# Kernel tuning notes

Measured on AMD Instinct MI355X. Metric: run time of the kernel, lower is better.

The kernel has to match this reference:

```python
import jax, jax.numpy as jnp
import numpy as np

EPS = 1e-16


def setup_inputs() -> dict:
    key = jax.random.key(0)
    k1, k2 = jax.random.split(key)
    p = jax.random.normal(k1, (2, 32, 2048, 4), dtype=jnp.float32)
    q = jax.random.normal(k2, (32, 2048, 4), dtype=jnp.float32)
    return {"p": p, "q": q}


def reference(p, q):
    # im=False path: take the real part of the complex generated momenta
    p_real = p[0]                      # (B, N, 4)
    # loss_norm_choice='p3', take_sqrt=True: use 3-momenta (drop energy)
    p3 = p_real[..., 1:]               # (B, N, 3)
    q3 = q[..., 1:]                    # (B, M, 3)
    # Pairwise Euclidean distance (cdist) via the expanded quadratic form to
    # avoid materializing the (B, N, M, 3) difference tensor.
    x2 = jnp.sum(p3 * p3, axis=-1)     # (B, N)
    y2 = jnp.sum(q3 * q3, axis=-1)     # (B, M)
    xy = jnp.einsum('bnd,bmd->bnm', p3, q3)  # (B, N, M)
    dist_sq = x2[..., :, None] + y2[..., None, :] - 2.0 * xy
    dist = jnp.sqrt(jnp.maximum(dist_sq, 0.0) + EPS)  # (B, N, M)
    # Bidirectional nearest-neighbor min-reduction
    min_pq = jnp.min(dist, axis=-1)    # (B, N)
    min_qp = jnp.min(dist, axis=-2)    # (B, M)
    chamfer_loss = jnp.sum((min_pq + min_qp) * 0.5)
    return chamfer_loss
```

## Files before the change

### kernel.cpp

```cpp
#include <hip/hip_runtime.h>
#include <math.h>


#define NPTS   2048
#define NBATCH 32
#define NTOT   (2 * NBATCH * NPTS)
#define EPSF   1e-16f
#define BIGF   3.4e38f

__device__ __forceinline__ float min3f(float a, float b, float c) {
    return fminf(fminf(a, b), c);
}

__global__ __launch_bounds__(256) void chamfer_tile_kernel(
    const float* __restrict__ P, const float* __restrict__ Q,
    unsigned int* __restrict__ ws)
{
    __shared__ float4 sp[256];
    __shared__ float4 sq[256];
    __shared__ float  scol[4][256];

    const int tid = threadIdx.x;
    const int tx  = tid & 15;
    const int ty  = tid >> 4;
    const int bi  = blockIdx.x;
    const int bj  = blockIdx.y;
    const int b   = blockIdx.z;

    {
        float4 pv = ((const float4*)P)[(size_t)b * NPTS + bi * 256 + tid];
        sp[tid] = make_float4(pv.y, pv.z, pv.w,
                              pv.y*pv.y + pv.z*pv.z + pv.w*pv.w);
        float4 qv = ((const float4*)Q)[(size_t)b * NPTS + bj * 256 + tid];
        sq[tid] = make_float4(-2.f*qv.y, -2.f*qv.z, -2.f*qv.w,
                              qv.y*qv.y + qv.z*qv.z + qv.w*qv.w);
    }
    __syncthreads();

    float px[16], py[16], pz[16], x2[16];
    #pragma unroll
    for (int k = 0; k < 16; ++k) {
        float4 v = sp[ty + 16 * k];
        px[k] = v.x; py[k] = v.y; pz[k] = v.z; x2[k] = v.w;
    }

    float rowacc[16], colacc[16];
    #pragma unroll
    for (int k = 0; k < 16; ++k) { rowacc[k] = BIGF; colacc[k] = BIGF; }

    for (int jp = 0; jp < 8; ++jp) {
        float4 q0 = sq[tx + 32 * jp];
        float4 q1 = sq[tx + 32 * jp + 16];
        float c0 = BIGF, c1 = BIGF;
        #pragma unroll
        for (int k = 0; k < 16; k += 2) {
            float t00 = fmaf(px[k],   q0.x, fmaf(py[k],   q0.y, pz[k]   * q0.z));
            float t01 = fmaf(px[k],   q1.x, fmaf(py[k],   q1.y, pz[k]   * q1.z));
            float t10 = fmaf(px[k+1], q0.x, fmaf(py[k+1], q0.y, pz[k+1] * q0.z));
            float t11 = fmaf(px[k+1], q1.x, fmaf(py[k+1], q1.y, pz[k+1] * q1.z));
            rowacc[k]   = min3f(rowacc[k],   t00 + q0.w, t01 + q1.w);
            rowacc[k+1] = min3f(rowacc[k+1], t10 + q0.w, t11 + q1.w);
            c0 = min3f(c0, t00 + x2[k], t10 + x2[k+1]);
            c1 = min3f(c1, t01 + x2[k], t11 + x2[k+1]);
        }
        colacc[2*jp]     = c0;
        colacc[2*jp + 1] = c1;
    }

    #pragma unroll
    for (int k = 0; k < 16; ++k) {
        float v = rowacc[k];
        v = fminf(v, __shfl_xor(v, 1));
        v = fminf(v, __shfl_xor(v, 2));
        v = fminf(v, __shfl_xor(v, 4));
        v = fminf(v, __shfl_xor(v, 8));
        rowacc[k] = v;
    }
    if (tx == 0) {
        #pragma unroll
        for (int k = 0; k < 16; ++k) {
            float d2 = fmaxf(x2[k] + rowacc[k], 0.f);
            atomicMin(&ws[b * NPTS + bi * 256 + (ty + 16 * k)],
                      __float_as_uint(d2));
        }
    }

    #pragma unroll
    for (int j = 0; j < 16; ++j) {
        float v = colacc[j];
        v = fminf(v, __shfl_xor(v, 16));
        v = fminf(v, __shfl_xor(v, 32));
        colacc[j] = v;
    }
    {
        const int wv   = tid >> 6;
        const int lane = tid & 63;
        if (lane < 16) {
            #pragma unroll
            for (int j = 0; j < 16; ++j) scol[wv][j * 16 + lane] = colacc[j];
        }
    }
    __syncthreads();
    {
        const int c = tid;
        float v = fminf(fminf(scol[0][c], scol[1][c]),
                        fminf(scol[2][c], scol[3][c]));
        float d2 = fmaxf(v + sq[c].w, 0.f);
        atomicMin(&ws[NBATCH * NPTS + b * NPTS + bj * 256 + c],
                  __float_as_uint(d2));
    }
}

__global__ __launch_bounds__(256) void chamfer_sum_kernel(
    const unsigned int* __restrict__ ws, float* __restrict__ out)
{
    __shared__ float rbuf[4];
    const int tid = threadIdx.x;
    const int i0  = blockIdx.x * 256 + tid;

    float s = 0.f;
    for (int i = i0; i < NTOT; i += gridDim.x * 256)
        s += sqrtf(__uint_as_float(ws[i]) + EPSF);

    #pragma unroll
    for (int off = 32; off > 0; off >>= 1) s += __shfl_down(s, off);
    if ((tid & 63) == 0) rbuf[tid >> 6] = s;
    __syncthreads();
    if (tid == 0)
        atomicAdd(out, 0.5f * ((rbuf[0] + rbuf[1]) + (rbuf[2] + rbuf[3])));
}

extern "C" void kernel_launch(void* const* d_in, const int* in_sizes, int n_in,
                              void* d_out, int out_size, void* d_ws, size_t ws_size,
                              hipStream_t stream) {
    const float* P = (const float*)d_in[0];
    const float* Q = (const float*)d_in[1];
    float* out = (float*)d_out;
    unsigned int* ws = (unsigned int*)d_ws;

    hipMemsetAsync(ws, 0x7F, (size_t)NTOT * sizeof(unsigned int), stream);
    hipMemsetAsync(out, 0, sizeof(float), stream);

    dim3 grid(NPTS / 256, NPTS / 256, NBATCH);
    chamfer_tile_kernel<<<grid, 256, 0, stream>>>(P, Q, ws);

    chamfer_sum_kernel<<<128, 256, 0, stream>>>(ws, out);
}
```

Baseline: 83.04 us.

## Stream all Q chunks per row block and replace atomics with partial-min buffers

Each block now owns 128 P rows and loops over all eight 256-point Q chunks with double-buffered shared memory. Row minima complete inside the block, so the row sqrt and sum happen in-kernel. Column minima go to a per-wave partial buffer without atomics, and a finish kernel reduces them and adds the row partial sums. This drops the workspace memset and the atomicMin traffic, at the cost of fewer blocks (512 instead of 2048), a serial loop per block, and a larger workspace read in the finish step.

```diff
diff --git a/kernel.cpp b/kernel.cpp
--- a/kernel.cpp
+++ b/kernel.cpp
@@ -4,7 +4,10 @@
 
 #define NPTS   2048
 #define NBATCH 32
-#define NTOT   (2 * NBATCH * NPTS)
+#define ROWCH  128
+#define NBI    (NPTS / ROWCH)
+#define NQCH   (NPTS / 256)
+#define COLPART_FLOATS ((size_t)NBATCH * NBI * 4 * NPTS)
 #define EPSF   1e-16f
 #define BIGF   3.4e38f
 
@@ -12,115 +15,130 @@
     return fminf(fminf(a, b), c);
 }
 
-__global__ __launch_bounds__(256) void chamfer_tile_kernel(
+__global__ __launch_bounds__(256) void chamfer_main_kernel(
     const float* __restrict__ P, const float* __restrict__ Q,
-    unsigned int* __restrict__ ws)
+    float* __restrict__ ws)
 {
-    __shared__ float4 sp[256];
-    __shared__ float4 sq[256];
-    __shared__ float  scol[4][256];
+    __shared__ float4 sq[2][256];
+    __shared__ float  rsum[4];
 
-    const int tid = threadIdx.x;
-    const int tx  = tid & 15;
-    const int ty  = tid >> 4;
-    const int bi  = blockIdx.x;
-    const int bj  = blockIdx.y;
-    const int b   = blockIdx.z;
+    const int tid  = threadIdx.x;
+    const int tx   = tid & 15;
+    const int ty   = tid >> 4;
+    const int lane = tid & 63;
+    const int wv   = tid >> 6;
+    const int bi   = blockIdx.x;
+    const int b    = blockIdx.y;
 
+    const float4* Pb = (const float4*)P + (size_t)b * NPTS + (size_t)bi * ROWCH;
+    float px[8], py[8], pz[8], x2[8], rowacc[8];
+    #pragma unroll
+    for (int k = 0; k < 8; ++k) {
+        float4 v = Pb[ty + 16 * k];
+        px[k] = v.y; py[k] = v.z; pz[k] = v.w;
+        x2[k] = v.y * v.y + v.z * v.z + v.w * v.w;
+        rowacc[k] = BIGF;
+    }
+
+    const float4* Qb = (const float4*)Q + (size_t)b * NPTS;
     {
-        float4 pv = ((const float4*)P)[(size_t)b * NPTS + bi * 256 + tid];
-        sp[tid] = make_float4(pv.y, pv.z, pv.w,
-                              pv.y*pv.y + pv.z*pv.z + pv.w*pv.w);
-        float4 qv = ((const float4*)Q)[(size_t)b * NPTS + bj * 256 + tid];
-        sq[tid] = make_float4(-2.f*qv.y, -2.f*qv.z, -2.f*qv.w,
-                              qv.y*qv.y + qv.z*qv.z + qv.w*qv.w);
+        float4 qv = Qb[tid];
+        sq[0][tid] = make_float4(-2.f * qv.y, -2.f * qv.z, -2.f * qv.w,
+                                 qv.y * qv.y + qv.z * qv.z + qv.w * qv.w);
     }
     __syncthreads();
 
-    float px[16], py[16], pz[16], x2[16];
-    #pragma unroll
-    for (int k = 0; k < 16; ++k) {
-        float4 v = sp[ty + 16 * k];
-        px[k] = v.x; py[k] = v.y; pz[k] = v.z; x2[k] = v.w;
+    float* colbase = ws + (((size_t)b * NBI + bi) * 4 + wv) * NPTS;
+
+    for (int jc = 0; jc < NQCH; ++jc) {
+        const int cur = jc & 1;
+        const bool have = (jc + 1 < NQCH);
+        float4 qnext;
+        if (have) qnext = Qb[(jc + 1) * 256 + tid];
+
+        float colv[16];
+        #pragma unroll
+        for (int jp = 0; jp < 8; ++jp) {
+            float4 q0 = sq[cur][tx + 32 * jp];
+            float4 q1 = sq[cur][tx + 32 * jp + 16];
+            float c0 = BIGF, c1 = BIGF;
+            #pragma unroll
+            for (int k = 0; k < 8; k += 2) {
+                float t00 = fmaf(px[k],   q0.x, fmaf(py[k],   q0.y, pz[k]   * q0.z));
+                float t01 = fmaf(px[k],   q1.x, fmaf(py[k],   q1.y, pz[k]   * q1.z));
+                float t10 = fmaf(px[k+1], q0.x, fmaf(py[k+1], q0.y, pz[k+1] * q0.z));
+                float t11 = fmaf(px[k+1], q1.x, fmaf(py[k+1], q1.y, pz[k+1] * q1.z));
+                rowacc[k]   = min3f(rowacc[k],   t00 + q0.w, t01 + q1.w);
+                rowacc[k+1] = min3f(rowacc[k+1], t10 + q0.w, t11 + q1.w);
+                c0 = min3f(c0, t00 + x2[k], t10 + x2[k+1]);
+                c1 = min3f(c1, t01 + x2[k], t11 + x2[k+1]);
+            }
+            colv[2*jp]     = c0;
+            colv[2*jp + 1] = c1;
+        }
+
+        #pragma unroll
+        for (int j = 0; j < 16; ++j) {
+            float v = colv[j];
+            v = fminf(v, __shfl_xor(v, 16));
+            v = fminf(v, __shfl_xor(v, 32));
+            colv[j] = v;
+        }
+        if (lane < 16) {
+            #pragma unroll
+            for (int j = 0; j < 16; ++j)
+                colbase[jc * 256 + j * 16 + lane] = colv[j];
+        }
+
+        if (have) {
+            sq[cur ^ 1][tid] = make_float4(
+                -2.f * qnext.y, -2.f * qnext.z, -2.f * qnext.w,
+                qnext.y * qnext.y + qnext.z * qnext.z + qnext.w * qnext.w);
+        }
+        __syncthreads();
     }
 
-    float rowacc[16], colacc[16];
+    float rs = 0.f;
     #pragma unroll
-    for (int k = 0; k < 16; ++k) { rowacc[k] = BIGF; colacc[k] = BIGF; }
-
-    for (int jp = 0; jp < 8; ++jp) {
-        float4 q0 = sq[tx + 32 * jp];
-        float4 q1 = sq[tx + 32 * jp + 16];
-        float c0 = BIGF, c1 = BIGF;
-        #pragma unroll
-        for (int k = 0; k < 16; k += 2) {
-            float t00 = fmaf(px[k],   q0.x, fmaf(py[k],   q0.y, pz[k]   * q0.z));
-            float t01 = fmaf(px[k],   q1.x, fmaf(py[k],   q1.y, pz[k]   * q1.z));
-            float t10 = fmaf(px[k+1], q0.x, fmaf(py[k+1], q0.y, pz[k+1] * q0.z));
-            float t11 = fmaf(px[k+1], q1.x, fmaf(py[k+1], q1.y, pz[k+1] * q1.z));
-            rowacc[k]   = min3f(rowacc[k],   t00 + q0.w, t01 + q1.w);
-            rowacc[k+1] = min3f(rowacc[k+1], t10 + q0.w, t11 + q1.w);
-            c0 = min3f(c0, t00 + x2[k], t10 + x2[k+1]);
-            c1 = min3f(c1, t01 + x2[k], t11 + x2[k+1]);
-        }
-        colacc[2*jp]     = c0;
-        colacc[2*jp + 1] = c1;
-    }
-
-    #pragma unroll
-    for (int k = 0; k < 16; ++k) {
+    for (int k = 0; k < 8; ++k) {
         float v = rowacc[k];
         v = fminf(v, __shfl_xor(v, 1));
         v = fminf(v, __shfl_xor(v, 2));
         v = fminf(v, __shfl_xor(v, 4));
         v = fminf(v, __shfl_xor(v, 8));
-        rowacc[k] = v;
+        rs += sqrtf(fmaxf(x2[k] + v, 0.f) + EPSF);
     }
-    if (tx == 0) {
-        #pragma unroll
-        for (int k = 0; k < 16; ++k) {
-            float d2 = fmaxf(x2[k] + rowacc[k], 0.f);
-            atomicMin(&ws[b * NPTS + bi * 256 + (ty + 16 * k)],
-                      __float_as_uint(d2));
-        }
-    }
-
-    #pragma unroll
-    for (int j = 0; j < 16; ++j) {
-        float v = colacc[j];
-        v = fminf(v, __shfl_xor(v, 16));
-        v = fminf(v, __shfl_xor(v, 32));
-        colacc[j] = v;
-    }
-    {
-        const int wv   = tid >> 6;
-        const int lane = tid & 63;
-        if (lane < 16) {
-            #pragma unroll
-            for (int j = 0; j < 16; ++j) scol[wv][j * 16 + lane] = colacc[j];
-        }
-    }
+    if (tx != 0) rs = 0.f;
+    rs += __shfl_xor(rs, 16);
+    rs += __shfl_xor(rs, 32);
+    if (lane == 0) rsum[wv] = rs;
     __syncthreads();
-    {
-        const int c = tid;
-        float v = fminf(fminf(scol[0][c], scol[1][c]),
-                        fminf(scol[2][c], scol[3][c]));
-        float d2 = fmaxf(v + sq[c].w, 0.f);
-        atomicMin(&ws[NBATCH * NPTS + b * NPTS + bj * 256 + c],
-                  __float_as_uint(d2));
-    }
+    if (tid == 0)
+        ws[COLPART_FLOATS + (size_t)b * NBI + bi] =
+            (rsum[0] + rsum[1]) + (rsum[2] + rsum[3]);
 }
 
-__global__ __launch_bounds__(256) void chamfer_sum_kernel(
-    const unsigned int* __restrict__ ws, float* __restrict__ out)
+__global__ __launch_bounds__(256) void chamfer_finish_kernel(
+    const float* __restrict__ ws, const float* __restrict__ Q,
+    float* __restrict__ out)
 {
     __shared__ float rbuf[4];
     const int tid = threadIdx.x;
-    const int i0  = blockIdx.x * 256 + tid;
+    const int b   = blockIdx.x >> 3;
+    const int cc  = blockIdx.x & 7;
+    const int col = cc * 256 + tid;
 
-    float s = 0.f;
-    for (int i = i0; i < NTOT; i += gridDim.x * 256)
-        s += sqrtf(__uint_as_float(ws[i]) + EPSF);
+    const float* base = ws + (size_t)b * NBI * 4 * NPTS + col;
+    float v = BIGF;
+    #pragma unroll
+    for (int i = 0; i < NBI * 4; ++i)
+        v = fminf(v, base[(size_t)i * NPTS]);
+
+    float4 qv = ((const float4*)Q)[(size_t)b * NPTS + col];
+    float y2 = qv.y * qv.y + qv.z * qv.z + qv.w * qv.w;
+    float s = sqrtf(fmaxf(v + y2, 0.f) + EPSF);
+
+    if (tid < 2) s += ws[COLPART_FLOATS + (size_t)blockIdx.x * 2 + tid];
 
     #pragma unroll
     for (int off = 32; off > 0; off >>= 1) s += __shfl_down(s, off);
@@ -136,13 +154,10 @@
     const float* P = (const float*)d_in[0];
     const float* Q = (const float*)d_in[1];
     float* out = (float*)d_out;
-    unsigned int* ws = (unsigned int*)d_ws;
+    float* ws  = (float*)d_ws;
 
-    hipMemsetAsync(ws, 0x7F, (size_t)NTOT * sizeof(unsigned int), stream);
     hipMemsetAsync(out, 0, sizeof(float), stream);
-
-    dim3 grid(NPTS / 256, NPTS / 256, NBATCH);
-    chamfer_tile_kernel<<<grid, 256, 0, stream>>>(P, Q, ws);
-
-    chamfer_sum_kernel<<<128, 256, 0, stream>>>(ws, out);
+    dim3 g1(NBI, NBATCH);
+    chamfer_main_kernel<<<g1, 256, 0, stream>>>(P, Q, ws);
+    chamfer_finish_kernel<<<256, 256, 0, stream>>>(ws, Q, out);
 }
```

Result: slower. 94.36 us (+13.6%).

## Replace atomicMin workspace with per-tile partial minima and smaller P tiles

Applied to the files above, without the earlier changes.

The tile kernel now covers 128 P rows by 256 Q columns, so the grid grows to 16x8x32 blocks. It writes per-tile partial row and column minima to distinct workspace slots instead of doing atomicMin into a shared array, which removes the workspace memset and the atomic traffic. P is loaded straight from global memory into registers, with no shared staging. The finish kernel then reduces the partials across tiles before the sqrt and sum. The cost is a larger workspace and extra reads in the finish kernel, and each thread now holds half as many P rows, which may lower register reuse per Q load.

```diff
diff --git a/kernel.cpp b/kernel.cpp
--- a/kernel.cpp
+++ b/kernel.cpp
@@ -4,7 +4,9 @@
 
 #define NPTS   2048
 #define NBATCH 32
-#define NTOT   (2 * NBATCH * NPTS)
+#define NBI    16
+#define NBJ    8
+#define WS_ROW_FLOATS ((size_t)NBATCH * NBI * NBJ * 128)
 #define EPSF   1e-16f
 #define BIGF   3.4e38f
 
@@ -14,46 +16,46 @@
 
 __global__ __launch_bounds__(256) void chamfer_tile_kernel(
     const float* __restrict__ P, const float* __restrict__ Q,
-    unsigned int* __restrict__ ws)
+    float* __restrict__ ws)
 {
-    __shared__ float4 sp[256];
     __shared__ float4 sq[256];
     __shared__ float  scol[4][256];
+    __shared__ float  rrow[128];
 
-    const int tid = threadIdx.x;
-    const int tx  = tid & 15;
-    const int ty  = tid >> 4;
-    const int bi  = blockIdx.x;
-    const int bj  = blockIdx.y;
-    const int b   = blockIdx.z;
+    const int tid  = threadIdx.x;
+    const int tx   = tid & 15;
+    const int ty   = tid >> 4;
+    const int lane = tid & 63;
+    const int wv   = tid >> 6;
+    const int bi   = blockIdx.x;
+    const int bj   = blockIdx.y;
+    const int b    = blockIdx.z;
 
     {
-        float4 pv = ((const float4*)P)[(size_t)b * NPTS + bi * 256 + tid];
-        sp[tid] = make_float4(pv.y, pv.z, pv.w,
-                              pv.y*pv.y + pv.z*pv.z + pv.w*pv.w);
         float4 qv = ((const float4*)Q)[(size_t)b * NPTS + bj * 256 + tid];
-        sq[tid] = make_float4(-2.f*qv.y, -2.f*qv.z, -2.f*qv.w,
-                              qv.y*qv.y + qv.z*qv.z + qv.w*qv.w);
+        sq[tid] = make_float4(-2.f * qv.y, -2.f * qv.z, -2.f * qv.w,
+                              qv.y * qv.y + qv.z * qv.z + qv.w * qv.w);
+    }
+
+    const float4* Pb = (const float4*)P + (size_t)b * NPTS + (size_t)bi * 128;
+    float px[8], py[8], pz[8], x2[8], rowacc[8];
+    #pragma unroll
+    for (int k = 0; k < 8; ++k) {
+        float4 v = Pb[ty + 16 * k];
+        px[k] = v.y; py[k] = v.z; pz[k] = v.w;
+        x2[k] = v.y * v.y + v.z * v.z + v.w * v.w;
+        rowacc[k] = BIGF;
     }
     __syncthreads();
 
-    float px[16], py[16], pz[16], x2[16];
+    float colacc[16];
     #pragma unroll
-    for (int k = 0; k < 16; ++k) {
-        float4 v = sp[ty + 16 * k];
-        px[k] = v.x; py[k] = v.y; pz[k] = v.z; x2[k] = v.w;
-    }
-
-    float rowacc[16], colacc[16];
-    #pragma unroll
-    for (int k = 0; k < 16; ++k) { rowacc[k] = BIGF; colacc[k] = BIGF; }
-
     for (int jp = 0; jp < 8; ++jp) {
         float4 q0 = sq[tx + 32 * jp];
         float4 q1 = sq[tx + 32 * jp + 16];
         float c0 = BIGF, c1 = BIGF;
         #pragma unroll
-        for (int k = 0; k < 16; k += 2) {
+        for (int k = 0; k < 8; k += 2) {
             float t00 = fmaf(px[k],   q0.x, fmaf(py[k],   q0.y, pz[k]   * q0.z));
             float t01 = fmaf(px[k],   q1.x, fmaf(py[k],   q1.y, pz[k]   * q1.z));
             float t10 = fmaf(px[k+1], q0.x, fmaf(py[k+1], q0.y, pz[k+1] * q0.z));
@@ -68,21 +70,13 @@
     }
 
     #pragma unroll
-    for (int k = 0; k < 16; ++k) {
+    for (int k = 0; k < 8; ++k) {
         float v = rowacc[k];
         v = fminf(v, __shfl_xor(v, 1));
         v = fminf(v, __shfl_xor(v, 2));
         v = fminf(v, __shfl_xor(v, 4));
         v = fminf(v, __shfl_xor(v, 8));
-        rowacc[k] = v;
-    }
-    if (tx == 0) {
-        #pragma unroll
-        for (int k = 0; k < 16; ++k) {
-            float d2 = fmaxf(x2[k] + rowacc[k], 0.f);
-            atomicMin(&ws[b * NPTS + bi * 256 + (ty + 16 * k)],
-                      __float_as_uint(d2));
-        }
+        if (tx == 0) rrow[ty + 16 * k] = x2[k] + v;
     }
 
     #pragma unroll
@@ -92,35 +86,50 @@
         v = fminf(v, __shfl_xor(v, 32));
         colacc[j] = v;
     }
-    {
-        const int wv   = tid >> 6;
-        const int lane = tid & 63;
-        if (lane < 16) {
-            #pragma unroll
-            for (int j = 0; j < 16; ++j) scol[wv][j * 16 + lane] = colacc[j];
-        }
+    if (lane < 16) {
+        #pragma unroll
+        for (int j = 0; j < 16; ++j) scol[wv][j * 16 + lane] = colacc[j];
     }
     __syncthreads();
+
     {
-        const int c = tid;
-        float v = fminf(fminf(scol[0][c], scol[1][c]),
-                        fminf(scol[2][c], scol[3][c]));
-        float d2 = fmaxf(v + sq[c].w, 0.f);
-        atomicMin(&ws[NBATCH * NPTS + b * NPTS + bj * 256 + c],
-                  __float_as_uint(d2));
+        float v = fminf(fminf(scol[0][tid], scol[1][tid]),
+                        fminf(scol[2][tid], scol[3][tid]));
+        float* wsC = ws + WS_ROW_FLOATS;
+        wsC[(((size_t)b * NBJ + bj) * NBI + bi) * 256 + tid] = v + sq[tid].w;
+    }
+    if (tid < 128) {
+        ws[(((size_t)b * NBI + bi) * NBJ + bj) * 128 + tid] = rrow[tid];
     }
 }
 
-__global__ __launch_bounds__(256) void chamfer_sum_kernel(
-    const unsigned int* __restrict__ ws, float* __restrict__ out)
+__global__ __launch_bounds__(256) void chamfer_finish_kernel(
+    const float* __restrict__ ws, float* __restrict__ out)
 {
     __shared__ float rbuf[4];
     const int tid = threadIdx.x;
-    const int i0  = blockIdx.x * 256 + tid;
+    const int i   = blockIdx.x * 256 + tid;
+    const int b   = i >> 11;
+    const int e   = i & 2047;
 
-    float s = 0.f;
-    for (int i = i0; i < NTOT; i += gridDim.x * 256)
-        s += sqrtf(__uint_as_float(ws[i]) + EPSF);
+    float s;
+    {
+        const int bi = e >> 7, rl = e & 127;
+        const float* rb = ws + ((size_t)(b * NBI + bi) * NBJ) * 128 + rl;
+        float v = BIGF;
+        #pragma unroll
+        for (int j = 0; j < NBJ; ++j) v = fminf(v, rb[j * 128]);
+        s = sqrtf(fmaxf(v, 0.f) + EPSF);
+    }
+    {
+        const int bj = e >> 8, cl = e & 255;
+        const float* cb = ws + WS_ROW_FLOATS
+                        + ((size_t)(b * NBJ + bj) * NBI) * 256 + cl;
+        float v = BIGF;
+        #pragma unroll
+        for (int j = 0; j < NBI; ++j) v = fminf(v, cb[j * 256]);
+        s += sqrtf(fmaxf(v, 0.f) + EPSF);
+    }
 
     #pragma unroll
     for (int off = 32; off > 0; off >>= 1) s += __shfl_down(s, off);
@@ -136,13 +145,10 @@
     const float* P = (const float*)d_in[0];
     const float* Q = (const float*)d_in[1];
     float* out = (float*)d_out;
-    unsigned int* ws = (unsigned int*)d_ws;
+    float* ws  = (float*)d_ws;
 
-    hipMemsetAsync(ws, 0x7F, (size_t)NTOT * sizeof(unsigned int), stream);
     hipMemsetAsync(out, 0, sizeof(float), stream);
-
-    dim3 grid(NPTS / 256, NPTS / 256, NBATCH);
+    dim3 grid(NBI, NBJ, NBATCH);
     chamfer_tile_kernel<<<grid, 256, 0, stream>>>(P, Q, ws);
-
-    chamfer_sum_kernel<<<128, 256, 0, stream>>>(ws, out);
+    chamfer_finish_kernel<<<256, 256, 0, stream>>>(ws, out);
 }
```

After: 100.8 us. 21.3% more time.
